# Kernel tuning notes

Hardware: AMD Instinct MI355X
Metric: run time of the kernel (lower is better)

The kernel has to match this reference:

```python
import jax, jax.numpy as jnp
import numpy as np

H = 200          # PREPARED_IMAGE_SIZE
BS = 8
NP = 64          # cloud points
HALF = H / 2.0   # image centre offset (100)


def _project_to_2d(cam_coeffs, points_3d, points_3d_base, points_2d_base):
    # points_3d: (bs, n, 3); cam_coeffs: (bs, 3cams, 2, 3) affine projection
    p3 = points_3d + points_3d_base[:, None]                       # (bs, n, 3)
    p2 = jnp.einsum('bcij,bnj->bcni', cam_coeffs, p3)              # (bs, 3, n, 2)
    return p2 - points_2d_base[:, :, None] + HALF


def _render_points(points, blur_sigmas):
    # points: (bs*3, n, 2) pixel coords; blur_sigmas: (bs, n)
    bs3, n, _ = points.shape
    bs = bs3 // 3
    pts = jnp.clip((points - 100.0) / 100.0, -1.0, 1.0)
    grid = jnp.linspace(-1.0, 1.0, H, dtype=jnp.float32)
    yv, xv = jnp.meshgrid(grid, grid, indexing='ij')
    m = jnp.stack([xv, yv], axis=-1)                               # (H, W, 2)
    diff = m[None, None] - pts[:, :, None, None, :]                # (bs3, n, H, W, 2)
    dst = diff[..., 0] ** 2 + diff[..., 1] ** 2                    # (bs3, n, H, W)
    sig = jnp.repeat(blur_sigmas, 3, axis=0)[:, :, None, None]     # (bs3, n, 1, 1)
    blobs = jnp.exp(-dst / (2.0 * sig ** 2))                       # (bs3, n, H, W)
    masks = jnp.minimum(blobs.sum(axis=1), 1.0)                    # (bs3, H, W)
    sum_ = jnp.maximum(masks.sum(axis=(1, 2), keepdims=True), 1e-8)
    masks_normed = (masks / sum_).reshape(bs, 3, H, H)
    blobs = blobs.reshape(bs, 3, n, H, H)
    return masks_normed, blobs


def setup_inputs() -> dict:
    key = jax.random.key(0)
    ks = jax.random.split(key, 6)
    cam_coeffs = jax.random.normal(ks[0], (BS, 3, 2, 3), dtype=jnp.float32) * 30.0
    cloud_points = jax.random.normal(ks[1], (BS, NP, 3), dtype=jnp.float32)
    masks_target = jax.random.uniform(ks[2], (BS, 3, H, H), dtype=jnp.float32)
    blur_sigmas_cloud = jax.random.uniform(ks[3], (BS, NP), dtype=jnp.float32) * 0.1 + 0.02
    points_3d_base = jax.random.normal(ks[4], (BS, 3), dtype=jnp.float32)
    points_2d_base = jax.random.normal(ks[5], (BS, 3, 2), dtype=jnp.float32)
    return {
        'cam_coeffs': cam_coeffs,
        'cloud_points': cloud_points,
        'masks_target': masks_target,
        'blur_sigmas_cloud': blur_sigmas_cloud,
        'points_3d_base': points_3d_base,
        'points_2d_base': points_2d_base,
    }


def reference(cam_coeffs, cloud_points, masks_target, blur_sigmas_cloud,
              points_3d_base, points_2d_base):
    bs = cam_coeffs.shape[0]
    p2d = _project_to_2d(cam_coeffs, cloud_points, points_3d_base, points_2d_base)
    masks_cloud, blobs = _render_points(p2d.reshape(bs * 3, NP, 2), blur_sigmas_cloud)
    # NOTE: normalization over dims (2,3) = (n_points, H), matching the torch source exactly
    sum_ = jnp.maximum(blobs.sum(axis=(2, 3), keepdims=True), 1e-8)
    blobs_normed = blobs / sum_
    scores = (blobs_normed * masks_target[:, :, None]).sum(axis=(3, 4)).mean(axis=1)
    return masks_cloud, scores
```

## Files before the change

### kernel.cpp

```cpp
#include <hip/hip_runtime.h>

#define H 200
#define NP 64
#define NIMG 24
#define NB 8
#define NPIX (H*H)
#define GSTEP (2.0f/199.0f)
#define SPI 20
#define NWORK (NIMG*SPI)

typedef __fp16 h2 __attribute__((ext_vector_type(2)));

__device__ __forceinline__ float fdot2f(unsigned int a, unsigned int b, float c) {
  h2 ha = __builtin_bit_cast(h2, a);
  h2 hb = __builtin_bit_cast(h2, b);
#if __has_builtin(__builtin_amdgcn_fdot2)
  return __builtin_amdgcn_fdot2(ha, hb, c, false);
#else
  return c + (float)ha.x * (float)hb.x + (float)ha.y * (float)hb.y;
#endif
}

__device__ __forceinline__ unsigned int pk2(float lo, float hi) {
#if __has_builtin(__builtin_amdgcn_cvt_pkrtz)
  h2 h = __builtin_amdgcn_cvt_pkrtz(lo, hi);
  return __builtin_bit_cast(unsigned int, h);
#else
  h2 h; h.x = (__fp16)lo; h.y = (__fp16)hi;
  return __builtin_bit_cast(unsigned int, h);
#endif
}

__global__ __launch_bounds__(256) void prs_main(
    const float* __restrict__ cam,
    const float* __restrict__ cloud,
    const float* __restrict__ mt,
    const float* __restrict__ blur,
    const float* __restrict__ b3,
    const float* __restrict__ b2,
    float* __restrict__ out,
    float* __restrict__ ws_msum,
    float* __restrict__ ws_scr)
{
  __shared__ float ex[NP*100];
  __shared__ float eys[20*NP];
  __shared__ unsigned int exp2_[32*100];
  __shared__ unsigned int eyp2[32*20];
  __shared__ unsigned int eyy[NP*12];
  __shared__ unsigned int Mp[100*12];
  __shared__ float cinv[100];
  __shared__ float Sy[NP];
  __shared__ float ptx[NP], pty[NP], i2s[NP];
  __shared__ float red[256];

  const int tid = threadIdx.x;
  const int blk = blockIdx.x;
  const int img = blk / SPI;
  const int rem = blk - img * SPI;
  const int strip = rem >> 1;
  const int xh = rem & 1;
  const int b = img / 3;
  const int c = img - 3 * b;
  const int ys0 = strip * 20;
  const int xb = xh * 100;

  if (tid < NP) {
    int n = tid;
    float p0 = cloud[(b*NP + n)*3 + 0] + b3[b*3 + 0];
    float p1 = cloud[(b*NP + n)*3 + 1] + b3[b*3 + 1];
    float p2 = cloud[(b*NP + n)*3 + 2] + b3[b*3 + 2];
    const float* cc = cam + ((b*3 + c)*2)*3;
    float px = cc[0]*p0 + cc[1]*p1 + cc[2]*p2 - b2[(b*3 + c)*2 + 0];
    float py = cc[3]*p0 + cc[4]*p1 + cc[5]*p2 - b2[(b*3 + c)*2 + 1];
    ptx[n] = fminf(fmaxf(px * 0.01f, -1.0f), 1.0f);
    pty[n] = fminf(fmaxf(py * 0.01f, -1.0f), 1.0f);
    float s = blur[b*NP + n];
    i2s[n] = 1.0f / (2.0f * s * s);
  }
  __syncthreads();

  for (int e = tid; e < 20*NP; e += 256) {
    int y = e >> 6, n = e & 63;
    float d = (-1.0f + (ys0 + y)*GSTEP) - pty[n];
    eys[y*NP + n] = __expf(-d*d*i2s[n]);
  }
  for (int e = tid; e < NP*100; e += 256) {
    int n = e / 100, x = e - n*100;
    float d = (-1.0f + (xb + x)*GSTEP) - ptx[n];
    ex[n*100 + x] = __expf(-d*d*i2s[n]);
  }
  {
    int n = tid & 63, g = tid >> 6;
    float pyv = pty[n], iv = i2s[n];
    float s = 0.0f;
    for (int y = g*50; y < g*50 + 50; ++y) {
      float d = (-1.0f + y*GSTEP) - pyv;
      s += __expf(-d*d*iv);
    }
    red[g*NP + n] = s;
  }
  __syncthreads();

  for (int e = tid; e < 3200; e += 256) {
    int n2 = e / 100, x = e - n2*100;
    exp2_[n2*100 + x] = pk2(ex[(2*n2)*100 + x], ex[(2*n2+1)*100 + x]);
  }
  for (int e = tid; e < 640; e += 256) {
    int n2 = e / 20, y = e - n2*20;
    eyp2[n2*20 + y] = pk2(eys[y*NP + 2*n2], eys[y*NP + 2*n2 + 1]);
  }
  for (int e = tid; e < 640; e += 256) {
    int n = e / 10, y2 = e - n*10;
    eyy[n*12 + y2] = pk2(eys[(2*y2)*NP + n], eys[(2*y2+1)*NP + n]);
  }
  for (int e = tid; e < 1000; e += 256) {
    int y2 = e / 100, x = e - y2*100;
    const float* mb = mt + img*NPIX + (ys0 + 2*y2)*H + xb + x;
    Mp[x*12 + y2] = pk2(mb[0], mb[H]);
  }
  if (tid < NP)
    Sy[tid] = red[tid] + red[NP + tid] + red[2*NP + tid] + red[3*NP + tid];
  __syncthreads();

  if (tid < 100) {
    float s = 0.0f;
    for (int n = 0; n < NP; ++n) s += ex[n*100 + tid] * Sy[n];
    cinv[tid] = 1.0f / fmaxf(s, 1e-8f);
  }
  __syncthreads();

  float msl = 0.0f;
  if (tid < 128) {
    if (tid < 125) {
      int yg = tid / 25;
      int xg = tid - yg*25;
      int x0 = xg*4, y0 = yg*4;
      float acc[4][4];
      #pragma unroll
      for (int i = 0; i < 4; ++i)
        #pragma unroll
        for (int j = 0; j < 4; ++j) acc[i][j] = 0.0f;
      for (int n2 = 0; n2 < 32; ++n2) {
        uint4 eyv = *(uint4*)&eyp2[n2*20 + y0];
        uint4 exv = *(uint4*)&exp2_[n2*100 + x0];
        acc[0][0]=fdot2f(eyv.x,exv.x,acc[0][0]); acc[0][1]=fdot2f(eyv.x,exv.y,acc[0][1]);
        acc[0][2]=fdot2f(eyv.x,exv.z,acc[0][2]); acc[0][3]=fdot2f(eyv.x,exv.w,acc[0][3]);
        acc[1][0]=fdot2f(eyv.y,exv.x,acc[1][0]); acc[1][1]=fdot2f(eyv.y,exv.y,acc[1][1]);
        acc[1][2]=fdot2f(eyv.y,exv.z,acc[1][2]); acc[1][3]=fdot2f(eyv.y,exv.w,acc[1][3]);
        acc[2][0]=fdot2f(eyv.z,exv.x,acc[2][0]); acc[2][1]=fdot2f(eyv.z,exv.y,acc[2][1]);
        acc[2][2]=fdot2f(eyv.z,exv.z,acc[2][2]); acc[2][3]=fdot2f(eyv.z,exv.w,acc[2][3]);
        acc[3][0]=fdot2f(eyv.w,exv.x,acc[3][0]); acc[3][1]=fdot2f(eyv.w,exv.y,acc[3][1]);
        acc[3][2]=fdot2f(eyv.w,exv.z,acc[3][2]); acc[3][3]=fdot2f(eyv.w,exv.w,acc[3][3]);
      }
      float* ob = out + img*NPIX;
      #pragma unroll
      for (int i = 0; i < 4; ++i) {
        float4 v;
        v.x = fminf(acc[i][0], 1.0f);
        v.y = fminf(acc[i][1], 1.0f);
        v.z = fminf(acc[i][2], 1.0f);
        v.w = fminf(acc[i][3], 1.0f);
        msl += v.x + v.y + v.z + v.w;
        *(float4*)&ob[(ys0 + y0 + i)*H + xb + x0] = v;
      }
    }
  } else {
    int st = tid - 128;
    int ng = st >> 3;
    int xt = st & 7;
    int n0 = ng * 4;
    uint4 ea[4], eb4[4]; uint2 ec[4];
    #pragma unroll
    for (int i = 0; i < 4; ++i) {
      const unsigned int* p = &eyy[(n0 + i)*12];
      ea[i]  = *(const uint4*)p;
      eb4[i] = *(const uint4*)(p + 4);
      ec[i]  = *(const uint2*)(p + 8);
    }
    float sacc[4] = {0.0f, 0.0f, 0.0f, 0.0f};
    for (int x = xt; x < 100; x += 8) {
      const unsigned int* q = &Mp[x*12];
      uint4 ma = *(const uint4*)q;
      uint4 mb = *(const uint4*)(q + 4);
      uint2 mc = *(const uint2*)(q + 8);
      float cvx = cinv[x];
      #pragma unroll
      for (int i = 0; i < 4; ++i) {
        float t = 0.0f;
        t = fdot2f(ea[i].x, ma.x, t);  t = fdot2f(ea[i].y, ma.y, t);
        t = fdot2f(ea[i].z, ma.z, t);  t = fdot2f(ea[i].w, ma.w, t);
        t = fdot2f(eb4[i].x, mb.x, t); t = fdot2f(eb4[i].y, mb.y, t);
        t = fdot2f(eb4[i].z, mb.z, t); t = fdot2f(eb4[i].w, mb.w, t);
        t = fdot2f(ec[i].x, mc.x, t);  t = fdot2f(ec[i].y, mc.y, t);
        sacc[i] += t * ex[(n0 + i)*100 + x] * cvx;
      }
    }
    #pragma unroll
    for (int off = 4; off > 0; off >>= 1) {
      #pragma unroll
      for (int i = 0; i < 4; ++i) sacc[i] += __shfl_down(sacc[i], off, 8);
    }
    if (xt == 0) {
      #pragma unroll
      for (int i = 0; i < 4; ++i) ws_scr[blk*NP + n0 + i] = sacc[i];
    }
  }

  red[tid] = msl;
  __syncthreads();
  #pragma unroll
  for (int s = 128; s > 0; s >>= 1) {
    if (tid < s) red[tid] += red[tid + s];
    __syncthreads();
  }
  if (tid == 0) ws_msum[blk] = red[0];
}

__global__ __launch_bounds__(256) void prs_finish(
    float* __restrict__ out,
    const float* __restrict__ ws_msum,
    const float* __restrict__ ws_scr)
{
  const int blk = blockIdx.x;
  const int tid = threadIdx.x;
  if (blk < NWORK) {
    const int img = blk / SPI;
    const int rem = blk - img * SPI;
    const int strip = rem >> 1;
    const int xh = rem & 1;
    __shared__ float invs;
    if (tid == 0) {
      float s = 0.0f;
      for (int i = 0; i < SPI; ++i) s += ws_msum[img*SPI + i];
      invs = 1.0f / fmaxf(s, 1e-8f);
    }
    __syncthreads();
    const float inv = invs;
    for (int q = tid; q < 500; q += 256) {
      int ry = q / 25;
      int rx = q - ry * 25;
      float* p = out + img*NPIX + (strip*20 + ry)*H + xh*100 + rx*4;
      float4 v = *(float4*)p;
      v.x *= inv; v.y *= inv; v.z *= inv; v.w *= inv;
      *(float4*)p = v;
    }
  } else {
    const int bb = blk - NWORK;
    if (tid < NP) {
      float s = 0.0f;
      for (int cc = 0; cc < 3; ++cc)
        for (int sh = 0; sh < SPI; ++sh)
          s += ws_scr[((bb*3 + cc)*SPI + sh)*NP + tid];
      out[NIMG*NPIX + bb*NP + tid] = s * (1.0f/3.0f);
    }
  }
}

extern "C" void kernel_launch(void* const* d_in, const int* in_sizes, int n_in,
                              void* d_out, int out_size, void* d_ws, size_t ws_size,
                              hipStream_t stream) {
  const float* cam   = (const float*)d_in[0];
  const float* cloud = (const float*)d_in[1];
  const float* mt    = (const float*)d_in[2];
  const float* blur  = (const float*)d_in[3];
  const float* b3    = (const float*)d_in[4];
  const float* b2    = (const float*)d_in[5];
  float* out = (float*)d_out;

  float* ws_msum = (float*)d_ws;
  float* ws_scr  = ws_msum + 512;

  prs_main<<<NWORK, 256, 0, stream>>>(cam, cloud, mt, blur, b3, b2,
                                      out, ws_msum, ws_scr);
  prs_finish<<<NWORK + NB, 256, 0, stream>>>(out, ws_msum, ws_scr);
}
```

Before: 20.73 us.

## Split per-image precompute into separate kernel and halve strip height

Adds a prs_pre kernel, one block per image. It computes the projected points, the inverse sigmas and the full-width column normalisers cinv once, instead of recomputing them in every strip block. The main kernel then uses 10-row strips, giving twice as many blocks with lighter per-block work and less shared memory. The mask product now uses fp32 FMAs on float4/float2 loads instead of packed fp16 dot products, and the block reduction uses wave shuffles. In exchange there is an extra kernel launch with a serial dependency, and the global workspace round-trip adds traffic.

Result: slower. 25.46 us (+22.8%).

```diff
diff --git a/kernel.cpp b/kernel.cpp
--- a/kernel.cpp
+++ b/kernel.cpp
@@ -6,7 +6,7 @@
 #define NB 8
 #define NPIX (H*H)
 #define GSTEP (2.0f/199.0f)
-#define SPI 20
+#define SPI 40
 #define NWORK (NIMG*SPI)
 
 typedef __fp16 h2 __attribute__((ext_vector_type(2)));
@@ -31,38 +31,23 @@
 #endif
 }
 
-__global__ __launch_bounds__(256) void prs_main(
+__global__ __launch_bounds__(256) void prs_pre(
     const float* __restrict__ cam,
     const float* __restrict__ cloud,
-    const float* __restrict__ mt,
     const float* __restrict__ blur,
     const float* __restrict__ b3,
     const float* __restrict__ b2,
-    float* __restrict__ out,
-    float* __restrict__ ws_msum,
-    float* __restrict__ ws_scr)
+    float* __restrict__ ws_pt,
+    float* __restrict__ ws_cinv)
 {
-  __shared__ float ex[NP*100];
-  __shared__ float eys[20*NP];
-  __shared__ unsigned int exp2_[32*100];
-  __shared__ unsigned int eyp2[32*20];
-  __shared__ unsigned int eyy[NP*12];
-  __shared__ unsigned int Mp[100*12];
-  __shared__ float cinv[100];
-  __shared__ float Sy[NP];
-  __shared__ float ptx[NP], pty[NP], i2s[NP];
+  __shared__ float ptx[NP], pty[NP], i2s[NP], Sy[NP];
   __shared__ float red[256];
+  __shared__ float cpart[800];
 
   const int tid = threadIdx.x;
-  const int blk = blockIdx.x;
-  const int img = blk / SPI;
-  const int rem = blk - img * SPI;
-  const int strip = rem >> 1;
-  const int xh = rem & 1;
+  const int img = blockIdx.x;
   const int b = img / 3;
-  const int c = img - 3 * b;
-  const int ys0 = strip * 20;
-  const int xb = xh * 100;
+  const int c = img - 3*b;
 
   if (tid < NP) {
     int n = tid;
@@ -72,23 +57,17 @@
     const float* cc = cam + ((b*3 + c)*2)*3;
     float px = cc[0]*p0 + cc[1]*p1 + cc[2]*p2 - b2[(b*3 + c)*2 + 0];
     float py = cc[3]*p0 + cc[4]*p1 + cc[5]*p2 - b2[(b*3 + c)*2 + 1];
-    ptx[n] = fminf(fmaxf(px * 0.01f, -1.0f), 1.0f);
-    pty[n] = fminf(fmaxf(py * 0.01f, -1.0f), 1.0f);
+    float pxv = fminf(fmaxf(px * 0.01f, -1.0f), 1.0f);
+    float pyv = fminf(fmaxf(py * 0.01f, -1.0f), 1.0f);
     float s = blur[b*NP + n];
-    i2s[n] = 1.0f / (2.0f * s * s);
-  }
-  __syncthreads();
-
-  for (int e = tid; e < 20*NP; e += 256) {
-    int y = e >> 6, n = e & 63;
-    float d = (-1.0f + (ys0 + y)*GSTEP) - pty[n];
-    eys[y*NP + n] = __expf(-d*d*i2s[n]);
-  }
-  for (int e = tid; e < NP*100; e += 256) {
-    int n = e / 100, x = e - n*100;
-    float d = (-1.0f + (xb + x)*GSTEP) - ptx[n];
-    ex[n*100 + x] = __expf(-d*d*i2s[n]);
-  }
+    float iv = 1.0f / (2.0f * s * s);
+    ptx[n] = pxv; pty[n] = pyv; i2s[n] = iv;
+    ws_pt[img*192 + n]       = pxv;
+    ws_pt[img*192 + 64 + n]  = pyv;
+    ws_pt[img*192 + 128 + n] = iv;
+  }
+  __syncthreads();
+
   {
     int n = tid & 63, g = tid >> 6;
     float pyv = pty[n], iv = i2s[n];
@@ -100,61 +79,116 @@
     red[g*NP + n] = s;
   }
   __syncthreads();
-
-  for (int e = tid; e < 3200; e += 256) {
-    int n2 = e / 100, x = e - n2*100;
-    exp2_[n2*100 + x] = pk2(ex[(2*n2)*100 + x], ex[(2*n2+1)*100 + x]);
-  }
+  if (tid < NP)
+    Sy[tid] = red[tid] + red[NP + tid] + red[2*NP + tid] + red[3*NP + tid];
+  __syncthreads();
+
+  for (int e = tid; e < 800; e += 256) {
+    int x = e >> 2, sub = e & 3;
+    float gx = -1.0f + x*GSTEP;
+    float s = 0.0f;
+    for (int k = 0; k < 16; ++k) {
+      int n = sub*16 + k;
+      float d = gx - ptx[n];
+      s += __expf(-d*d*i2s[n]) * Sy[n];
+    }
+    cpart[e] = s;
+  }
+  __syncthreads();
+  if (tid < 200) {
+    float s = cpart[tid*4] + cpart[tid*4+1] + cpart[tid*4+2] + cpart[tid*4+3];
+    ws_cinv[img*200 + tid] = 1.0f / fmaxf(s, 1e-8f);
+  }
+}
+
+__global__ __launch_bounds__(256, 4) void prs_main(
+    const float* __restrict__ mt,
+    const float* __restrict__ ws_pt,
+    const float* __restrict__ ws_cinv,
+    float* __restrict__ out,
+    float* __restrict__ ws_msum,
+    float* __restrict__ ws_scr)
+{
+  __shared__ float ex[NP*100];
+  __shared__ float eys[10*NP];
+  __shared__ float eyt[NP*12];
+  __shared__ unsigned int eyy[NP*8];
+  __shared__ unsigned int Mp[100*8];
+  __shared__ float cinv[100];
+  __shared__ float ptx[NP], pty[NP], i2s[NP];
+  __shared__ float red2[2];
+
+  const int tid = threadIdx.x;
+  const int blk = blockIdx.x;
+  const int img = blk / SPI;
+  const int rem = blk - img * SPI;
+  const int strip = rem >> 1;
+  const int xh = rem & 1;
+  const int ys0 = strip * 10;
+  const int xb = xh * 100;
+
+  if (tid < NP) {
+    ptx[tid] = ws_pt[img*192 + tid];
+    pty[tid] = ws_pt[img*192 + 64 + tid];
+    i2s[tid] = ws_pt[img*192 + 128 + tid];
+  }
+  if (tid >= 128 && tid < 228) cinv[tid - 128] = ws_cinv[img*200 + xb + (tid - 128)];
+  __syncthreads();
+
+  for (int e = tid; e < 10*NP; e += 256) {
+    int y = e >> 6, n = e & 63;
+    float d = (-1.0f + (ys0 + y)*GSTEP) - pty[n];
+    eys[y*NP + n] = __expf(-d*d*i2s[n]);
+  }
+  {
+    int n = tid >> 2;
+    int x0 = (tid & 3) * 25;
+    float pxv = ptx[n], iv = i2s[n];
+    for (int k = 0; k < 25; ++k) {
+      int x = x0 + k;
+      float d = (-1.0f + (xb + x)*GSTEP) - pxv;
+      ex[n*100 + x] = __expf(-d*d*iv);
+    }
+  }
+  __syncthreads();
+
   for (int e = tid; e < 640; e += 256) {
-    int n2 = e / 20, y = e - n2*20;
-    eyp2[n2*20 + y] = pk2(eys[y*NP + 2*n2], eys[y*NP + 2*n2 + 1]);
-  }
-  for (int e = tid; e < 640; e += 256) {
-    int n = e / 10, y2 = e - n*10;
-    eyy[n*12 + y2] = pk2(eys[(2*y2)*NP + n], eys[(2*y2+1)*NP + n]);
-  }
-  for (int e = tid; e < 1000; e += 256) {
+    int n = e / 10, y = e - n*10;
+    eyt[n*12 + y] = eys[y*NP + n];
+  }
+  for (int e = tid; e < 320; e += 256) {
+    int n = e / 5, y2 = e - n*5;
+    eyy[n*8 + y2] = pk2(eys[(2*y2)*NP + n], eys[(2*y2+1)*NP + n]);
+  }
+  for (int e = tid; e < 500; e += 256) {
     int y2 = e / 100, x = e - y2*100;
     const float* mb = mt + img*NPIX + (ys0 + 2*y2)*H + xb + x;
-    Mp[x*12 + y2] = pk2(mb[0], mb[H]);
-  }
-  if (tid < NP)
-    Sy[tid] = red[tid] + red[NP + tid] + red[2*NP + tid] + red[3*NP + tid];
-  __syncthreads();
-
-  if (tid < 100) {
-    float s = 0.0f;
-    for (int n = 0; n < NP; ++n) s += ex[n*100 + tid] * Sy[n];
-    cinv[tid] = 1.0f / fmaxf(s, 1e-8f);
-  }
-  __syncthreads();
-
-  float msl = 0.0f;
+    Mp[x*8 + y2] = pk2(mb[0], mb[H]);
+  }
+  __syncthreads();
+
   if (tid < 128) {
+    float msl = 0.0f;
     if (tid < 125) {
       int yg = tid / 25;
       int xg = tid - yg*25;
-      int x0 = xg*4, y0 = yg*4;
-      float acc[4][4];
-      #pragma unroll
-      for (int i = 0; i < 4; ++i)
+      int y0 = yg*2, x0 = xg*4;
+      float acc[2][4];
+      #pragma unroll
+      for (int i = 0; i < 2; ++i)
         #pragma unroll
         for (int j = 0; j < 4; ++j) acc[i][j] = 0.0f;
-      for (int n2 = 0; n2 < 32; ++n2) {
-        uint4 eyv = *(uint4*)&eyp2[n2*20 + y0];
-        uint4 exv = *(uint4*)&exp2_[n2*100 + x0];
-        acc[0][0]=fdot2f(eyv.x,exv.x,acc[0][0]); acc[0][1]=fdot2f(eyv.x,exv.y,acc[0][1]);
-        acc[0][2]=fdot2f(eyv.x,exv.z,acc[0][2]); acc[0][3]=fdot2f(eyv.x,exv.w,acc[0][3]);
-        acc[1][0]=fdot2f(eyv.y,exv.x,acc[1][0]); acc[1][1]=fdot2f(eyv.y,exv.y,acc[1][1]);
-        acc[1][2]=fdot2f(eyv.y,exv.z,acc[1][2]); acc[1][3]=fdot2f(eyv.y,exv.w,acc[1][3]);
-        acc[2][0]=fdot2f(eyv.z,exv.x,acc[2][0]); acc[2][1]=fdot2f(eyv.z,exv.y,acc[2][1]);
-        acc[2][2]=fdot2f(eyv.z,exv.z,acc[2][2]); acc[2][3]=fdot2f(eyv.z,exv.w,acc[2][3]);
-        acc[3][0]=fdot2f(eyv.w,exv.x,acc[3][0]); acc[3][1]=fdot2f(eyv.w,exv.y,acc[3][1]);
-        acc[3][2]=fdot2f(eyv.w,exv.z,acc[3][2]); acc[3][3]=fdot2f(eyv.w,exv.w,acc[3][3]);
+      for (int n = 0; n < NP; ++n) {
+        float4 exv = *(float4*)&ex[n*100 + x0];
+        float2 eyv = *(float2*)&eyt[n*12 + y0];
+        acc[0][0] += eyv.x*exv.x; acc[0][1] += eyv.x*exv.y;
+        acc[0][2] += eyv.x*exv.z; acc[0][3] += eyv.x*exv.w;
+        acc[1][0] += eyv.y*exv.x; acc[1][1] += eyv.y*exv.y;
+        acc[1][2] += eyv.y*exv.z; acc[1][3] += eyv.y*exv.w;
       }
       float* ob = out + img*NPIX;
       #pragma unroll
-      for (int i = 0; i < 4; ++i) {
+      for (int i = 0; i < 2; ++i) {
         float4 v;
         v.x = fminf(acc[i][0], 1.0f);
         v.y = fminf(acc[i][1], 1.0f);
@@ -164,34 +198,33 @@
         *(float4*)&ob[(ys0 + y0 + i)*H + xb + x0] = v;
       }
     }
+    #pragma unroll
+    for (int off = 32; off > 0; off >>= 1) msl += __shfl_down(msl, off);
+    if ((tid & 63) == 0) red2[tid >> 6] = msl;
   } else {
     int st = tid - 128;
     int ng = st >> 3;
     int xt = st & 7;
     int n0 = ng * 4;
-    uint4 ea[4], eb4[4]; uint2 ec[4];
+    uint4 ea[4]; unsigned int ec[4];
     #pragma unroll
     for (int i = 0; i < 4; ++i) {
-      const unsigned int* p = &eyy[(n0 + i)*12];
-      ea[i]  = *(const uint4*)p;
-      eb4[i] = *(const uint4*)(p + 4);
-      ec[i]  = *(const uint2*)(p + 8);
+      ea[i] = *(const uint4*)&eyy[(n0 + i)*8];
+      ec[i] = eyy[(n0 + i)*8 + 4];
     }
     float sacc[4] = {0.0f, 0.0f, 0.0f, 0.0f};
     for (int x = xt; x < 100; x += 8) {
-      const unsigned int* q = &Mp[x*12];
-      uint4 ma = *(const uint4*)q;
-      uint4 mb = *(const uint4*)(q + 4);
-      uint2 mc = *(const uint2*)(q + 8);
+      uint4 ma = *(const uint4*)&Mp[x*8];
+      unsigned int mc = Mp[x*8 + 4];
       float cvx = cinv[x];
       #pragma unroll
       for (int i = 0; i < 4; ++i) {
         float t = 0.0f;
-        t = fdot2f(ea[i].x, ma.x, t);  t = fdot2f(ea[i].y, ma.y, t);
-        t = fdot2f(ea[i].z, ma.z, t);  t = fdot2f(ea[i].w, ma.w, t);
-        t = fdot2f(eb4[i].x, mb.x, t); t = fdot2f(eb4[i].y, mb.y, t);
-        t = fdot2f(eb4[i].z, mb.z, t); t = fdot2f(eb4[i].w, mb.w, t);
-        t = fdot2f(ec[i].x, mc.x, t);  t = fdot2f(ec[i].y, mc.y, t);
+        t = fdot2f(ea[i].x, ma.x, t);
+        t = fdot2f(ea[i].y, ma.y, t);
+        t = fdot2f(ea[i].z, ma.z, t);
+        t = fdot2f(ea[i].w, ma.w, t);
+        t = fdot2f(ec[i],   mc,   t);
         sacc[i] += t * ex[(n0 + i)*100 + x] * cvx;
       }
     }
@@ -205,15 +238,8 @@
       for (int i = 0; i < 4; ++i) ws_scr[blk*NP + n0 + i] = sacc[i];
     }
   }
-
-  red[tid] = msl;
-  __syncthreads();
-  #pragma unroll
-  for (int s = 128; s > 0; s >>= 1) {
-    if (tid < s) red[tid] += red[tid + s];
-    __syncthreads();
-  }
-  if (tid == 0) ws_msum[blk] = red[0];
+  __syncthreads();
+  if (tid == 0) ws_msum[blk] = red2[0] + red2[1];
 }
 
 __global__ __launch_bounds__(256) void prs_finish(
@@ -223,9 +249,9 @@
 {
   const int blk = blockIdx.x;
   const int tid = threadIdx.x;
-  if (blk < NWORK) {
-    const int img = blk / SPI;
-    const int rem = blk - img * SPI;
+  if (blk < 480) {
+    const int img = blk / 20;
+    const int rem = blk - img * 20;
     const int strip = rem >> 1;
     const int xh = rem & 1;
     __shared__ float invs;
@@ -245,7 +271,7 @@
       *(float4*)p = v;
     }
   } else {
-    const int bb = blk - NWORK;
+    const int bb = blk - 480;
     if (tid < NP) {
       float s = 0.0f;
       for (int cc = 0; cc < 3; ++cc)
@@ -268,9 +294,11 @@
   float* out = (float*)d_out;
 
   float* ws_msum = (float*)d_ws;
-  float* ws_scr  = ws_msum + 512;
-
-  prs_main<<<NWORK, 256, 0, stream>>>(cam, cloud, mt, blur, b3, b2,
-                                      out, ws_msum, ws_scr);
-  prs_finish<<<NWORK + NB, 256, 0, stream>>>(out, ws_msum, ws_scr);
-}
+  float* ws_scr  = ws_msum + 1024;
+  float* ws_pt   = ws_scr + NWORK*NP;
+  float* ws_cinv = ws_pt + NIMG*192;
+
+  prs_pre<<<NIMG, 256, 0, stream>>>(cam, cloud, blur, b3, b2, ws_pt, ws_cinv);
+  prs_main<<<NWORK, 256, 0, stream>>>(mt, ws_pt, ws_cinv, out, ws_msum, ws_scr);
+  prs_finish<<<488, 256, 0, stream>>>(out, ws_msum, ws_scr);
+}
```
